# Kernel tuning notes

Measured on AMD Instinct MI355X. Metric: run time of the kernel, lower is better.

Reference implementation:

```python
import jax, jax.numpy as jnp
import numpy as np

N = 200_000   # nodes
E = 6_400_000 # edges (avg degree 32)


def setup_inputs() -> dict:
    key = jax.random.key(0)
    k = jax.random.split(key, 6)
    x = jax.random.normal(k[0], (N, 2), dtype=jnp.float32)
    edge_index = jax.random.randint(k[1], (2, E), 0, N, dtype=jnp.int32)
    # GCNConv(2, 8) and GCNConv(8, 4) parameters (Glorot-ish init, zero bias as in PyG)
    W1 = jax.random.normal(k[2], (2, 8), dtype=jnp.float32) * (1.0 / np.sqrt(2.0))
    b1 = jnp.zeros((8,), dtype=jnp.float32)
    W2 = jax.random.normal(k[3], (8, 4), dtype=jnp.float32) * (1.0 / np.sqrt(8.0))
    b2 = jnp.zeros((4,), dtype=jnp.float32)
    return {"x": x, "edge_index": edge_index, "W1": W1, "b1": b1, "W2": W2, "b2": b2}


def _gcn_conv(x, src, dst, norm, W, b, n):
    # PyG GCNConv: linear transform, normalized gather/scatter-add, bias after aggregation
    h = x @ W                                   # [N, F_out]
    msg = h[src] * norm[:, None]                # gather + edge-wise scale, [E', F_out]
    agg = jax.ops.segment_sum(msg, dst, num_segments=n)  # scatter-add at targets
    return agg + b


def reference(x, edge_index, W1, b1, W2, b2):
    n = x.shape[0]
    # add self-loops (PyG default add_self_loops=True)
    loops = jnp.arange(n, dtype=edge_index.dtype)
    src = jnp.concatenate([edge_index[0], loops])
    dst = jnp.concatenate([edge_index[1], loops])
    # symmetric degree normalization: deg computed at targets with unit edge weights
    deg = jax.ops.segment_sum(jnp.ones_like(src, dtype=x.dtype), dst, num_segments=n)
    deg_inv_sqrt = jnp.where(deg > 0, jax.lax.rsqrt(jnp.maximum(deg, 1.0)), 0.0)
    norm = deg_inv_sqrt[src] * deg_inv_sqrt[dst]  # [E']

    h = jax.nn.relu(_gcn_conv(x, src, dst, norm, W1, b1, n))
    out = _gcn_conv(h, src, dst, norm, W2, b2, n)
    return out
```

## Files before the change

kernel.cpp:

```cpp
#include <hip/hip_runtime.h>


#define EPB   8192
#define PART  2048
#define LPBIT 11
#define SRCB  18
#define BC    4
#define RSTR  2049
#define STCAP 17408
#define NSL1  256
#define CAP1  2304
#define NSL2  128
#define CAP2  1280


__global__ __launch_bounds__(512) void countA_kernel(
    const int* __restrict__ dst, int* __restrict__ cntmat, int E, int P) {
    __shared__ int cnt[128];
    int tid = threadIdx.x;
    if (tid < 128) cnt[tid] = 0;
    __syncthreads();
    int nv4 = E >> 2;
    int b4 = (blockIdx.x * EPB) >> 2;
    int e4 = min(b4 + (EPB >> 2), nv4);
    const int4* d4 = (const int4*)dst;
    #pragma unroll
    for (int k = 0; k < (EPB >> 2); k += 512) {
        int i = b4 + k + tid;
        if (i < e4) {
            int4 d = d4[i];
            atomicAdd(&cnt[d.x >> LPBIT], 1);
            atomicAdd(&cnt[d.y >> LPBIT], 1);
            atomicAdd(&cnt[d.z >> LPBIT], 1);
            atomicAdd(&cnt[d.w >> LPBIT], 1);
        }
    }
    if (blockIdx.x == gridDim.x - 1) {
        int e = (nv4 << 2) + tid;
        if (e < E) atomicAdd(&cnt[dst[e] >> LPBIT], 1);
    }
    __syncthreads();
    int* row = cntmat + (size_t)blockIdx.x * P;
    if (tid < P) row[tid] = cnt[tid];
}

__global__ __launch_bounds__(256) void colscanA_kernel(
    int* __restrict__ cntmat, int* __restrict__ colTotal, int B, int P) {
    __shared__ int sdata[256];
    int p = blockIdx.x, tid = threadIdx.x;
    int v[4];
    int s = 0;
    #pragma unroll
    for (int k = 0; k < 4; k++) {
        int b = tid * 4 + k;
        v[k] = (b < B) ? cntmat[(size_t)b * P + p] : 0;
        s += v[k];
    }
    int x = s;
    sdata[tid] = x;
    __syncthreads();
    for (int off = 1; off < 256; off <<= 1) {
        int t = (tid >= off) ? sdata[tid - off] : 0;
        __syncthreads();
        x += t;
        sdata[tid] = x;
        __syncthreads();
    }
    int run = x - s;
    #pragma unroll
    for (int k = 0; k < 4; k++) {
        int b = tid * 4 + k;
        if (b < B) cntmat[(size_t)b * P + p] = run;
        run += v[k];
    }
    if (tid == 255) colTotal[p] = x;
}

__global__ __launch_bounds__(256) void totalscanA_kernel(
    const int* __restrict__ colTotal, int* __restrict__ colStart,
    int P, int E) {
    __shared__ int sdata[256];
    int tid = threadIdx.x;
    int v[4];
    int s = 0;
    #pragma unroll
    for (int k = 0; k < 4; k++) {
        int i = tid * 4 + k;
        v[k] = (i < P) ? colTotal[i] : 0;
        s += v[k];
    }
    int x = s;
    sdata[tid] = x;
    __syncthreads();
    for (int off = 1; off < 256; off <<= 1) {
        int t = (tid >= off) ? sdata[tid - off] : 0;
        __syncthreads();
        x += t;
        sdata[tid] = x;
        __syncthreads();
    }
    int run = x - s;
    #pragma unroll
    for (int k = 0; k < 4; k++) {
        int i = tid * 4 + k;
        if (i < P) colStart[i] = run;
        run += v[k];
    }
    if (tid == 0) colStart[P] = E;
}

__global__ __launch_bounds__(512) void scatterA_kernel(
    const int* __restrict__ src, const int* __restrict__ dst,
    const int* __restrict__ cntmat, const int* __restrict__ colStart,
    unsigned* __restrict__ packed, int E, int P) {
    __shared__ int cur[128];
    int tid = threadIdx.x;
    if (tid < P) cur[tid] = colStart[tid] + cntmat[(size_t)blockIdx.x * P + tid];
    __syncthreads();
    int nv4 = E >> 2;
    int b4 = (blockIdx.x * EPB) >> 2;
    int e4 = min(b4 + (EPB >> 2), nv4);
    const int4* d4 = (const int4*)dst;
    const int4* s4 = (const int4*)src;
    #pragma unroll
    for (int k = 0; k < (EPB >> 2); k += 512) {
        int i = b4 + k + tid;
        if (i < e4) {
            int4 d = d4[i];
            int4 sv = s4[i];
            int p0 = atomicAdd(&cur[d.x >> LPBIT], 1);
            packed[p0] = ((unsigned)(d.x & (PART - 1)) << SRCB) | (unsigned)sv.x;
            int p1 = atomicAdd(&cur[d.y >> LPBIT], 1);
            packed[p1] = ((unsigned)(d.y & (PART - 1)) << SRCB) | (unsigned)sv.y;
            int p2 = atomicAdd(&cur[d.z >> LPBIT], 1);
            packed[p2] = ((unsigned)(d.z & (PART - 1)) << SRCB) | (unsigned)sv.z;
            int p3 = atomicAdd(&cur[d.w >> LPBIT], 1);
            packed[p3] = ((unsigned)(d.w & (PART - 1)) << SRCB) | (unsigned)sv.w;
        }
    }
    if (blockIdx.x == gridDim.x - 1) {
        int e = (nv4 << 2) + tid;
        if (e < E) {
            int d = dst[e];
            int pos = atomicAdd(&cur[d >> LPBIT], 1);
            packed[pos] = ((unsigned)(d & (PART - 1)) << SRCB) | (unsigned)src[e];
        }
    }
}


__global__ __launch_bounds__(512) void localC_kernel(
    const unsigned* __restrict__ packed, const int* __restrict__ colStart,
    int* __restrict__ runStart, int* __restrict__ srcsorted) {
    __shared__ int hist[PART];
    __shared__ int sdata[512];
    __shared__ unsigned stage[STCAP];
    int tid = threadIdx.x;
    int dp = blockIdx.x >> 2, b = blockIdx.x & (BC - 1);
    int s0 = colStart[dp], len = colStart[dp + 1] - s0;
    int lo = s0 + (int)(((long long)len * b) / BC);
    int hi = s0 + (int)(((long long)len * (b + 1)) / BC);
    for (int k = tid; k < PART; k += 512) hist[k] = 0;
    __syncthreads();
    for (int i = lo + tid; i < hi; i += 512)
        atomicAdd(&hist[packed[i] >> SRCB], 1);
    __syncthreads();
    int off = tid * 4;
    int v0 = hist[off], v1 = hist[off + 1], v2 = hist[off + 2], v3 = hist[off + 3];
    int s = v0 + v1 + v2 + v3;
    int x = s;
    sdata[tid] = x;
    __syncthreads();
    for (int o = 1; o < 512; o <<= 1) {
        int t = (tid >= o) ? sdata[tid - o] : 0;
        __syncthreads();
        x += t;
        sdata[tid] = x;
        __syncthreads();
    }
    int run = x - s;
    int* rs = runStart + (size_t)(dp * BC + b) * RSTR;
    int c0 = lo + run, c1 = c0 + v0, c2 = c1 + v1, c3 = c2 + v2;
    rs[off] = c0; rs[off + 1] = c1; rs[off + 2] = c2; rs[off + 3] = c3;
    __syncthreads();
    hist[off] = c0; hist[off + 1] = c1; hist[off + 2] = c2; hist[off + 3] = c3;
    if (tid == 0) rs[PART] = hi;
    __syncthreads();
    int total = hi - lo;
    bool ovf = total > STCAP;
    for (int i = lo + tid; i < hi; i += 512) {
        unsigned w = packed[i];
        int pos = atomicAdd(&hist[w >> SRCB], 1);
        unsigned sv = w & ((1u << SRCB) - 1);
        if (!ovf) stage[pos - lo] = sv;
        else srcsorted[pos] = (int)sv;
    }
    __syncthreads();
    if (!ovf)
        for (int j = tid; j < total; j += 512) srcsorted[lo + j] = (int)stage[j];
}


__global__ __launch_bounds__(512) void dinvg_kernel(
    const int* __restrict__ runStart, const float* __restrict__ x,
    float* __restrict__ dinv, float* __restrict__ g, int n) {
    int i = blockIdx.x * 512 + threadIdx.x;
    if (i >= n) return;
    int dp = i >> LPBIT, ld = i & (PART - 1);
    int deg = 0;
    #pragma unroll
    for (int b = 0; b < BC; b++) {
        const int* rs = runStart + (size_t)(dp * BC + b) * RSTR + ld;
        deg += rs[1] - rs[0];
    }
    float d = rsqrtf((float)deg + 1.0f);
    dinv[i] = d;
    float2 xv = ((const float2*)x)[i];
    ((float2*)g)[i] = make_float2(xv.x * d, xv.y * d);
}


__global__ __launch_bounds__(512) void agg1p_kernel(
    const int* __restrict__ srcsorted, const int* __restrict__ runStart,
    const float* __restrict__ g, float* __restrict__ partial1) {
    __shared__ float2 stage[CAP1];
    __shared__ int srs[NSL1 + 1];
    int tid = threadIdx.x;
    int bid = blockIdx.x;
    int sl = bid & 7, rb = bid >> 3;
    const int* rs = runStart + (size_t)rb * RSTR + sl * NSL1;
    if (tid <= NSL1) srs[tid] = rs[tid];
    __syncthreads();
    int lo = srs[0], hi = srs[NSL1];
    const float2* gp = (const float2*)g;
    bool ovf = (hi - lo) > CAP1;
    if (!ovf)
        for (int e = lo + tid; e < hi; e += 512)
            stage[e - lo] = gp[srcsorted[e]];
    __syncthreads();
    int nid = tid >> 1, c = tid & 1;
    int a = srs[nid] - lo, bnd = srs[nid + 1] - lo;
    float acc = 0.0f;
    if (!ovf) {
        const float* st = (const float*)stage;
        for (int j = a; j < bnd; j++) acc += st[j * 2 + c];
    } else {
        for (int j = a; j < bnd; j++)
            acc += g[2 * (size_t)srcsorted[lo + j] + c];
    }
    partial1[(size_t)bid * 512 + tid] = acc;
}

__global__ __launch_bounds__(512) void combine1_kernel(
    const float* __restrict__ partial1, const float* __restrict__ g,
    const float* __restrict__ dinv, const float* __restrict__ W1,
    const float* __restrict__ b1, const float* __restrict__ W2,
    float* __restrict__ hs2, int n) {
    int i = blockIdx.x * 512 + threadIdx.x;
    if (i >= n) return;
    int dp = i >> LPBIT, ld = i & (PART - 1);
    int sl = ld >> 8, off = ld & (NSL1 - 1);
    float s0 = 0.0f, s1 = 0.0f;
    #pragma unroll
    for (int b = 0; b < BC; b++) {
        int bid = ((dp * BC + b) << 3) | sl;
        const float* q = partial1 + (size_t)bid * 512 + off * 2;
        s0 += q[0];
        s1 += q[1];
    }
    float d = dinv[i];
    float2 gi = ((const float2*)g)[i];
    s0 = (s0 + gi.x) * d;
    s1 = (s1 + gi.y) * d;
    float oc0 = 0.0f, oc1 = 0.0f, oc2 = 0.0f, oc3 = 0.0f;
    #pragma unroll
    for (int f = 0; f < 8; f++) {
        float h = fmaxf(s0 * W1[f] + s1 * W1[8 + f] + b1[f], 0.0f);
        oc0 += h * W2[4 * f];
        oc1 += h * W2[4 * f + 1];
        oc2 += h * W2[4 * f + 2];
        oc3 += h * W2[4 * f + 3];
    }
    float4 o;
    o.x = oc0 * d; o.y = oc1 * d; o.z = oc2 * d; o.w = oc3 * d;
    ((float4*)hs2)[i] = o;
}

__global__ __launch_bounds__(512) void agg2p_kernel(
    const int* __restrict__ srcsorted, const int* __restrict__ runStart,
    const float* __restrict__ hs2, float* __restrict__ partial2) {
    __shared__ float4 stage[CAP2];
    __shared__ int srs[NSL2 + 1];
    int tid = threadIdx.x;
    int bid = blockIdx.x;
    int sl = bid & 15, rb = bid >> 4;
    const int* rs = runStart + (size_t)rb * RSTR + sl * NSL2;
    if (tid <= NSL2) srs[tid] = rs[tid];
    __syncthreads();
    int lo = srs[0], hi = srs[NSL2];
    const float4* hp = (const float4*)hs2;
    bool ovf = (hi - lo) > CAP2;
    if (!ovf)
        for (int e = lo + tid; e < hi; e += 512)
            stage[e - lo] = hp[srcsorted[e]];
    __syncthreads();
    int nid = tid >> 2, c = tid & 3;
    int a = srs[nid] - lo, bnd = srs[nid + 1] - lo;
    float acc = 0.0f;
    if (!ovf) {
        const float* st = (const float*)stage;
        for (int j = a; j < bnd; j++) acc += st[j * 4 + c];
    } else {
        for (int j = a; j < bnd; j++)
            acc += hs2[4 * (size_t)srcsorted[lo + j] + c];
    }
    partial2[(size_t)bid * 512 + tid] = acc;
}

__global__ __launch_bounds__(512) void combine2_kernel(
    const float* __restrict__ partial2, const float* __restrict__ hs2,
    const float* __restrict__ dinv, const float* __restrict__ b2,
    float* __restrict__ out, int n) {
    int i = blockIdx.x * 512 + threadIdx.x;
    if (i >= n) return;
    int dp = i >> LPBIT, ld = i & (PART - 1);
    int sl = ld >> 7, off = ld & (NSL2 - 1);
    float s0 = 0.0f, s1 = 0.0f, s2 = 0.0f, s3 = 0.0f;
    #pragma unroll
    for (int b = 0; b < BC; b++) {
        int bid = ((dp * BC + b) << 4) | sl;
        const float* q = partial2 + (size_t)bid * 512 + off * 4;
        s0 += q[0];
        s1 += q[1];
        s2 += q[2];
        s3 += q[3];
    }
    float d = dinv[i];
    float4 hv = ((const float4*)hs2)[i];
    float4 o;
    o.x = d * (s0 + hv.x) + b2[0];
    o.y = d * (s1 + hv.y) + b2[1];
    o.z = d * (s2 + hv.z) + b2[2];
    o.w = d * (s3 + hv.w) + b2[3];
    ((float4*)out)[i] = o;
}

extern "C" void kernel_launch(void* const* d_in, const int* in_sizes, int n_in,
                              void* d_out, int out_size, void* d_ws, size_t ws_size,
                              hipStream_t stream) {
    const float* x   = (const float*)d_in[0];
    const int*   ei  = (const int*)d_in[1];
    const float* W1  = (const float*)d_in[2];
    const float* b1  = (const float*)d_in[3];
    const float* W2  = (const float*)d_in[4];
    const float* b2  = (const float*)d_in[5];
    float* out = (float*)d_out;

    const int n = in_sizes[0] / 2;
    const int E = in_sizes[1] / 2;
    const int* src = ei;
    const int* dst = ei + E;

    const int P  = (n + PART - 1) >> LPBIT;
    const int B1 = (E + EPB - 1) / EPB;

    int* ws = (int*)d_ws;
    int* colTotal = ws;
    int* colStart = ws + 1024;
    int* cntmatA  = ws + 2048;
    size_t cmsz = (((size_t)B1 * P) + 3) & ~(size_t)3;
    int* runStart = cntmatA + cmsz;
    size_t rssz = (((size_t)P * BC * RSTR) + 3) & ~(size_t)3;
    unsigned* packed = (unsigned*)(runStart + rssz);
    int* srcsorted = (int*)(packed + E);
    size_t nd = (size_t)P << LPBIT;
    float* dinv = (float*)packed;
    float* g    = dinv + nd;
    float* hs2  = g + 2 * nd;
    float* partial = hs2 + 4 * nd;

    const int gN  = (n + 511) / 512;
    const int gA1 = P * BC * (PART / NSL1);
    const int gA2 = P * BC * (PART / NSL2);

    countA_kernel    <<<B1, 512, 0, stream>>>(dst, cntmatA, E, P);
    colscanA_kernel  <<<P, 256, 0, stream>>>(cntmatA, colTotal, B1, P);
    totalscanA_kernel<<<1, 256, 0, stream>>>(colTotal, colStart, P, E);
    scatterA_kernel  <<<B1, 512, 0, stream>>>(src, dst, cntmatA, colStart, packed, E, P);
    localC_kernel    <<<P * BC, 512, 0, stream>>>(packed, colStart, runStart, srcsorted);
    dinvg_kernel     <<<gN, 512, 0, stream>>>(runStart, x, dinv, g, n);
    agg1p_kernel     <<<gA1, 512, 0, stream>>>(srcsorted, runStart, g, partial);
    combine1_kernel  <<<gN, 512, 0, stream>>>(partial, g, dinv, W1, b1, W2, hs2, n);
    agg2p_kernel     <<<gA2, 512, 0, stream>>>(srcsorted, runStart, hs2, partial);
    combine2_kernel  <<<gN, 512, 0, stream>>>(partial, hs2, dinv, b2, out, n);
}
```

Before: 244.6 us.

## Fuse aggregation and combine kernels by looping over edge buckets per block

```diff
diff --git a/kernel.cpp b/kernel.cpp
--- a/kernel.cpp
+++ b/kernel.cpp
@@ -220,129 +220,103 @@
 }
 
 
-__global__ __launch_bounds__(512) void agg1p_kernel(
+__global__ __launch_bounds__(512) void agg1f_kernel(
     const int* __restrict__ srcsorted, const int* __restrict__ runStart,
-    const float* __restrict__ g, float* __restrict__ partial1) {
+    const float* __restrict__ g, const float* __restrict__ dinv,
+    const float* __restrict__ W1, const float* __restrict__ b1,
+    const float* __restrict__ W2, float* __restrict__ hs2, int n) {
     __shared__ float2 stage[CAP1];
     __shared__ int srs[NSL1 + 1];
-    int tid = threadIdx.x;
-    int bid = blockIdx.x;
-    int sl = bid & 7, rb = bid >> 3;
-    const int* rs = runStart + (size_t)rb * RSTR + sl * NSL1;
-    if (tid <= NSL1) srs[tid] = rs[tid];
-    __syncthreads();
-    int lo = srs[0], hi = srs[NSL1];
+    __shared__ float sres[NSL1][2];
+    int tid = threadIdx.x;
+    int dp = blockIdx.x >> 3, sl = blockIdx.x & 7;
+    int nid = tid >> 1, c = tid & 1;
     const float2* gp = (const float2*)g;
-    bool ovf = (hi - lo) > CAP1;
-    if (!ovf)
-        for (int e = lo + tid; e < hi; e += 512)
-            stage[e - lo] = gp[srcsorted[e]];
-    __syncthreads();
-    int nid = tid >> 1, c = tid & 1;
-    int a = srs[nid] - lo, bnd = srs[nid + 1] - lo;
     float acc = 0.0f;
-    if (!ovf) {
-        const float* st = (const float*)stage;
-        for (int j = a; j < bnd; j++) acc += st[j * 2 + c];
-    } else {
-        for (int j = a; j < bnd; j++)
-            acc += g[2 * (size_t)srcsorted[lo + j] + c];
-    }
-    partial1[(size_t)bid * 512 + tid] = acc;
-}
-
-__global__ __launch_bounds__(512) void combine1_kernel(
-    const float* __restrict__ partial1, const float* __restrict__ g,
-    const float* __restrict__ dinv, const float* __restrict__ W1,
-    const float* __restrict__ b1, const float* __restrict__ W2,
-    float* __restrict__ hs2, int n) {
-    int i = blockIdx.x * 512 + threadIdx.x;
-    if (i >= n) return;
-    int dp = i >> LPBIT, ld = i & (PART - 1);
-    int sl = ld >> 8, off = ld & (NSL1 - 1);
-    float s0 = 0.0f, s1 = 0.0f;
     #pragma unroll
     for (int b = 0; b < BC; b++) {
-        int bid = ((dp * BC + b) << 3) | sl;
-        const float* q = partial1 + (size_t)bid * 512 + off * 2;
-        s0 += q[0];
-        s1 += q[1];
-    }
-    float d = dinv[i];
-    float2 gi = ((const float2*)g)[i];
-    s0 = (s0 + gi.x) * d;
-    s1 = (s1 + gi.y) * d;
-    float oc0 = 0.0f, oc1 = 0.0f, oc2 = 0.0f, oc3 = 0.0f;
-    #pragma unroll
-    for (int f = 0; f < 8; f++) {
-        float h = fmaxf(s0 * W1[f] + s1 * W1[8 + f] + b1[f], 0.0f);
-        oc0 += h * W2[4 * f];
-        oc1 += h * W2[4 * f + 1];
-        oc2 += h * W2[4 * f + 2];
-        oc3 += h * W2[4 * f + 3];
-    }
-    float4 o;
-    o.x = oc0 * d; o.y = oc1 * d; o.z = oc2 * d; o.w = oc3 * d;
-    ((float4*)hs2)[i] = o;
-}
-
-__global__ __launch_bounds__(512) void agg2p_kernel(
+        const int* rs = runStart + (size_t)(dp * BC + b) * RSTR + sl * NSL1;
+        if (tid <= NSL1) srs[tid] = rs[tid];
+        __syncthreads();
+        int lo = srs[0], hi = srs[NSL1];
+        bool ovf = (hi - lo) > CAP1;
+        if (!ovf)
+            for (int e = lo + tid; e < hi; e += 512)
+                stage[e - lo] = gp[srcsorted[e]];
+        __syncthreads();
+        int a = srs[nid] - lo, bnd = srs[nid + 1] - lo;
+        if (!ovf) {
+            const float* st = (const float*)stage;
+            for (int j = a; j < bnd; j++) acc += st[j * 2 + c];
+        } else {
+            for (int j = a; j < bnd; j++)
+                acc += g[2 * (size_t)srcsorted[lo + j] + c];
+        }
+        __syncthreads();
+    }
+    sres[nid][c] = acc;
+    __syncthreads();
+    if (tid < NSL1) {
+        int i = ((dp << LPBIT) | (sl * NSL1)) + tid;
+        if (i < n) {
+            float d = dinv[i];
+            float2 gi = gp[i];
+            float s0 = (sres[tid][0] + gi.x) * d;
+            float s1 = (sres[tid][1] + gi.y) * d;
+            float oc0 = 0.0f, oc1 = 0.0f, oc2 = 0.0f, oc3 = 0.0f;
+            #pragma unroll
+            for (int f = 0; f < 8; f++) {
+                float h = fmaxf(s0 * W1[f] + s1 * W1[8 + f] + b1[f], 0.0f);
+                oc0 += h * W2[4 * f];
+                oc1 += h * W2[4 * f + 1];
+                oc2 += h * W2[4 * f + 2];
+                oc3 += h * W2[4 * f + 3];
+            }
+            float4 o;
+            o.x = oc0 * d; o.y = oc1 * d; o.z = oc2 * d; o.w = oc3 * d;
+            ((float4*)hs2)[i] = o;
+        }
+    }
+}
+
+__global__ __launch_bounds__(512) void agg2f_kernel(
     const int* __restrict__ srcsorted, const int* __restrict__ runStart,
-    const float* __restrict__ hs2, float* __restrict__ partial2) {
+    const float* __restrict__ hs2, const float* __restrict__ dinv,
+    const float* __restrict__ b2, float* __restrict__ out, int n) {
     __shared__ float4 stage[CAP2];
     __shared__ int srs[NSL2 + 1];
     int tid = threadIdx.x;
-    int bid = blockIdx.x;
-    int sl = bid & 15, rb = bid >> 4;
-    const int* rs = runStart + (size_t)rb * RSTR + sl * NSL2;
-    if (tid <= NSL2) srs[tid] = rs[tid];
-    __syncthreads();
-    int lo = srs[0], hi = srs[NSL2];
+    int dp = blockIdx.x >> 4, sl = blockIdx.x & 15;
+    int nid = tid >> 2, c = tid & 3;
     const float4* hp = (const float4*)hs2;
-    bool ovf = (hi - lo) > CAP2;
-    if (!ovf)
-        for (int e = lo + tid; e < hi; e += 512)
-            stage[e - lo] = hp[srcsorted[e]];
-    __syncthreads();
-    int nid = tid >> 2, c = tid & 3;
-    int a = srs[nid] - lo, bnd = srs[nid + 1] - lo;
     float acc = 0.0f;
-    if (!ovf) {
-        const float* st = (const float*)stage;
-        for (int j = a; j < bnd; j++) acc += st[j * 4 + c];
-    } else {
-        for (int j = a; j < bnd; j++)
-            acc += hs2[4 * (size_t)srcsorted[lo + j] + c];
-    }
-    partial2[(size_t)bid * 512 + tid] = acc;
-}
-
-__global__ __launch_bounds__(512) void combine2_kernel(
-    const float* __restrict__ partial2, const float* __restrict__ hs2,
-    const float* __restrict__ dinv, const float* __restrict__ b2,
-    float* __restrict__ out, int n) {
-    int i = blockIdx.x * 512 + threadIdx.x;
-    if (i >= n) return;
-    int dp = i >> LPBIT, ld = i & (PART - 1);
-    int sl = ld >> 7, off = ld & (NSL2 - 1);
-    float s0 = 0.0f, s1 = 0.0f, s2 = 0.0f, s3 = 0.0f;
     #pragma unroll
     for (int b = 0; b < BC; b++) {
-        int bid = ((dp * BC + b) << 4) | sl;
-        const float* q = partial2 + (size_t)bid * 512 + off * 4;
-        s0 += q[0];
-        s1 += q[1];
-        s2 += q[2];
-        s3 += q[3];
-    }
-    float d = dinv[i];
-    float4 hv = ((const float4*)hs2)[i];
-    float4 o;
-    o.x = d * (s0 + hv.x) + b2[0];
-    o.y = d * (s1 + hv.y) + b2[1];
-    o.z = d * (s2 + hv.z) + b2[2];
-    o.w = d * (s3 + hv.w) + b2[3];
-    ((float4*)out)[i] = o;
+        const int* rs = runStart + (size_t)(dp * BC + b) * RSTR + sl * NSL2;
+        if (tid <= NSL2) srs[tid] = rs[tid];
+        __syncthreads();
+        int lo = srs[0], hi = srs[NSL2];
+        bool ovf = (hi - lo) > CAP2;
+        if (!ovf)
+            for (int e = lo + tid; e < hi; e += 512)
+                stage[e - lo] = hp[srcsorted[e]];
+        __syncthreads();
+        int a = srs[nid] - lo, bnd = srs[nid + 1] - lo;
+        if (!ovf) {
+            const float* st = (const float*)stage;
+            for (int j = a; j < bnd; j++) acc += st[j * 4 + c];
+        } else {
+            for (int j = a; j < bnd; j++)
+                acc += hs2[4 * (size_t)srcsorted[lo + j] + c];
+        }
+        __syncthreads();
+    }
+    int i = ((dp << LPBIT) | (sl * NSL2)) + nid;
+    if (i < n) {
+        float d = dinv[i];
+        float hv = hs2[4 * (size_t)i + c];
+        out[4 * (size_t)i + c] = d * (acc + hv) + b2[c];
+    }
 }
 
 extern "C" void kernel_launch(void* const* d_in, const int* in_sizes, int n_in,
@@ -377,11 +351,10 @@
     float* dinv = (float*)packed;
     float* g    = dinv + nd;
     float* hs2  = g + 2 * nd;
-    float* partial = hs2 + 4 * nd;
 
     const int gN  = (n + 511) / 512;
-    const int gA1 = P * BC * (PART / NSL1);
-    const int gA2 = P * BC * (PART / NSL2);
+    const int gA1 = P * (PART / NSL1);
+    const int gA2 = P * (PART / NSL2);
 
     countA_kernel    <<<B1, 512, 0, stream>>>(dst, cntmatA, E, P);
     colscanA_kernel  <<<P, 256, 0, stream>>>(cntmatA, colTotal, B1, P);
@@ -389,8 +362,6 @@
     scatterA_kernel  <<<B1, 512, 0, stream>>>(src, dst, cntmatA, colStart, packed, E, P);
     localC_kernel    <<<P * BC, 512, 0, stream>>>(packed, colStart, runStart, srcsorted);
     dinvg_kernel     <<<gN, 512, 0, stream>>>(runStart, x, dinv, g, n);
-    agg1p_kernel     <<<gA1, 512, 0, stream>>>(srcsorted, runStart, g, partial);
-    combine1_kernel  <<<gN, 512, 0, stream>>>(partial, g, dinv, W1, b1, W2, hs2, n);
-    agg2p_kernel     <<<gA2, 512, 0, stream>>>(srcsorted, runStart, hs2, partial);
-    combine2_kernel  <<<gN, 512, 0, stream>>>(partial, hs2, dinv, b2, out, n);
-}
+    agg1f_kernel     <<<gA1, 512, 0, stream>>>(srcsorted, runStart, g, dinv, W1, b1, W2, hs2, n);
+    agg2f_kernel     <<<gA2, 512, 0, stream>>>(srcsorted, runStart, hs2, dinv, b2, out, n);
+}
```

Result: faster. 235.0 us (-3.9%).
